# Performance work log

Measured on AMD Instinct MI355X. Metric: run time of the kernel, lower is better.

## Reference

```python
import jax, jax.numpy as jnp
import numpy as np

N = 116                      # AAL atlas nodes
E = N * (N - 1) // 2         # 6670 edges of the fully connected connectome
HID = 64
EDIM = 5
OUT = 4
ENC = HID + N // 2           # 122 raw brain-encoding features
EPS = 1e-10


def setup_inputs() -> dict:
    key = jax.random.key(0)
    ks = jax.random.split(key, 15)
    iu = np.triu_indices(N, k=1)                      # matches torch.nonzero(triu) order
    edge_index = jnp.asarray(np.stack(iu), dtype=jnp.int32)   # [2, E]
    rn = lambda k, s, sc=0.1: jax.random.normal(k, s, dtype=jnp.float32) * sc
    return dict(
        encoding_raw=rn(ks[0], (N, ENC), 1.0),
        edge_attr=rn(ks[1], (E, EDIM), 1.0),
        edge_index=edge_index,
        W_enc=rn(ks[2], (ENC, HID)), b_enc=rn(ks[3], (HID,)),
        W1=rn(ks[4], (HID, HID)), b1=rn(ks[5], (HID,)), p1=rn(ks[6], (1, EDIM)),
        We=rn(ks[7], (EDIM, EDIM)), be=rn(ks[8], (EDIM,)), pe=rn(ks[9], (1, HID)),
        W2=rn(ks[10], (HID, HID)), b2=rn(ks[11], (HID,)), p2=rn(ks[12], (1, EDIM)),
        Wl=rn(ks[13], (HID, OUT)), bl=rn(ks[14], (OUT,)),
    )


def _forward(encoding_raw, edge_attr, edge_index, W_enc, b_enc,
             W1, b1, p1, We, be, pe, W2, b2, p2, Wl, bl):
    eye_n = jnp.eye(N, dtype=jnp.float32)
    eye_e = jnp.eye(E, dtype=jnp.float32)
    adj_v = 1.0 - eye_n          # fully-connected node adjacency, zero diagonal
    adj_e = 1.0 - eye_e          # edge adjacency: ones minus eye
    # Incidence matrix T [N, E]: T[i,e] = T[j,e] = 1 for edge e = (i, j)
    cols = jnp.arange(E)
    T = (jnp.zeros((N, E), dtype=jnp.float32)
         .at[edge_index[0], cols].set(1.0)
         .at[edge_index[1], cols].set(1.0))

    # BrainEncoding: x = Linear(raw encoding)  (batch.x is None -> x = encodings)
    x = encoding_raw @ W_enc + b_enc                    # [N, HID]

    def node_conv(Hv, He, W, b, p):
        d = (He @ p.T)[:, 0]                            # [E] learned scalar per edge
        mult = (T * d) @ T.T                            # T diag(d) T^T  -> [N, N]
        # M1 = eye*1 + (1-eye)*mult, then * adj_v (zero diag) => mult * adj_v
        A = mult * adj_v
        return A @ (Hv @ W) + b

    def edge_conv(Hv, He, W, b, p):
        dv = (Hv @ p.T)[:, 0]                           # [N] learned scalar per node
        mult = T.T @ (dv[:, None] * T)                  # T^T diag(dv) T -> [E, E] dense
        A = mult * adj_e                                # M3 * adj_e => zero diag, off-diag mult
        A = A / (A.max(axis=0, keepdims=True) + EPS)    # column-max normalization
        return A @ (He @ W) + b

    # node_conv1 -> relu (dropout is identity in eval)
    x = jax.nn.relu(node_conv(x, edge_attr, W1, b1, p1))
    e = jax.nn.relu(edge_attr)
    # edge_conv1 -> relu
    e = jax.nn.relu(edge_conv(x, e, We, be, pe))
    x = jax.nn.relu(x)                                  # relu applied again (idempotent)
    # node_conv2 (no relu after)
    x = node_conv(x, e, W2, b2, p2)
    # global mean pool over the single graph, then classifier head
    pooled = jnp.mean(x, axis=0, keepdims=True)         # [1, HID]
    return pooled @ Wl + bl                             # [1, OUT]


def reference(encoding_raw, edge_attr, edge_index, W_enc, b_enc,
              W1, b1, p1, We, be, pe, W2, b2, p2, Wl, bl):
    return _forward(encoding_raw, edge_attr, edge_index, W_enc, b_enc,
                    W1, b1, p1, We, be, pe, W2, b2, p2, Wl, bl)
```

## Files before the change

kernel.cpp:

```cpp
#include <hip/hip_runtime.h>


#define NN   116
#define EE   6670
#define HID  64
#define EDIM 5
#define OUTD 4
#define ENC  122
#define EPSF 1e-10f
#define NH   (NN*HID)

__device__ __forceinline__ int eid_ij(int i, int j) {
    int a = i < j ? i : j;
    int b = i < j ? j : i;
    return a*NN - ((a*(a+1)) >> 1) + (b - a - 1);
}

__global__ __launch_bounds__(256) void kA(
    const float* __restrict__ enc, const float* __restrict__ ea,
    const float* __restrict__ W_enc, const float* __restrict__ b_enc,
    const float* __restrict__ p1, const float* __restrict__ We,
    const float* __restrict__ W1,
    float* __restrict__ Y1, float* __restrict__ d1, float* __restrict__ G)
{
    const int tid = threadIdx.x;
    if (blockIdx.x < 29) {
        __shared__ __align__(16) float sWe[ENC*HID];
        __shared__ __align__(16) float sW1[HID*HID];
        __shared__ __align__(16) float sEnc[4*ENC];
        __shared__ float sX[4*HID];
        {
            const float4* g4 = (const float4*)W_enc; float4* s4 = (float4*)sWe;
            for (int u = tid; u < ENC*HID/4; u += 256) s4[u] = g4[u];
        }
        {
            const float4* g4 = (const float4*)W1; float4* s4 = (float4*)sW1;
            for (int u = tid; u < HID*HID/4; u += 256) s4[u] = g4[u];
        }
        {
            const float4* g4 = (const float4*)(enc + blockIdx.x*4*ENC);
            float4* s4 = (float4*)sEnc;
            for (int u = tid; u < 4*ENC/4; u += 256) s4[u] = g4[u];
        }
        __syncthreads();
        const int w = tid >> 6, h = tid & 63;
        const int i = blockIdx.x*4 + w;
        float acc = b_enc[h];
        const float* er = sEnc + w*ENC;
        #pragma unroll 4
        for (int k = 0; k < ENC; ++k) acc = fmaf(er[k], sWe[k*HID + h], acc);
        sX[w*HID + h] = acc;
        __syncthreads();
        float a2 = 0.f;
        const float* xr = sX + w*HID;
        #pragma unroll 8
        for (int k = 0; k < HID; ++k) a2 = fmaf(xr[k], sW1[k*HID + h], a2);
        Y1[i*HID + h] = a2;
    } else {
        int u = (blockIdx.x - 29)*256 + tid;
        if (u < EE) {
            const float* r = ea + u*EDIM;
            float a0 = 0.f;
            #pragma unroll
            for (int k = 0; k < EDIM; ++k) a0 = fmaf(r[k], p1[k], a0);
            d1[u] = a0;
        } else if (u < EE + EE*EDIM) {
            int idx = u - EE;
            int e = idx / EDIM, k = idx - e*EDIM;
            const float* r = ea + e*EDIM;
            float a0 = 0.f;
            #pragma unroll
            for (int m = 0; m < EDIM; ++m) a0 = fmaf(fmaxf(r[m], 0.f), We[m*EDIM + k], a0);
            G[idx] = a0;
        }
    }
}

__global__ __launch_bounds__(256) void kB(
    const float* __restrict__ d1, const float* __restrict__ Y1,
    const float* __restrict__ b1, const float* __restrict__ pe,
    const float* __restrict__ W2,
    float* __restrict__ dv, float* __restrict__ Y2)
{
    __shared__ __align__(16) float sY[NH];
    __shared__ __align__(16) float sD[EE];
    __shared__ float sX2[4*HID];
    const int tid = threadIdx.x;
    {
        const float4* g4 = (const float4*)Y1; float4* s4 = (float4*)sY;
        for (int u = tid; u < NH/4; u += 256) s4[u] = g4[u];
        const float2* g2 = (const float2*)d1; float2* s2 = (float2*)sD;
        for (int u = tid; u < EE/2; u += 256) s2[u] = g2[u];
    }
    __syncthreads();
    const int w = tid >> 6, h = tid & 63;
    const int i = blockIdx.x*4 + w;
    float acc = b1[h];
    #pragma unroll 4
    for (int j = 0; j < NN; ++j) {
        int jj = (j == i) ? (j ^ 1) : j;
        float wgt = (j == i) ? 0.f : sD[eid_ij(i, jj)];
        acc = fmaf(wgt, sY[jj*HID + h], acc);
    }
    float v = fmaxf(acc, 0.f);
    float r = v * pe[h];
    #pragma unroll
    for (int off = 32; off > 0; off >>= 1) r += __shfl_down(r, off, 64);
    if (h == 0) dv[i] = r;
    sX2[w*HID + h] = v;
    __syncthreads();
    float a2 = 0.f;
    const float* xr = sX2 + w*HID;
    #pragma unroll 8
    for (int k = 0; k < HID; ++k) a2 = fmaf(xr[k], W2[k*HID + h], a2);
    Y2[i*HID + h] = a2;
}

__global__ __launch_bounds__(256) void kC(
    const float* __restrict__ G, const float* __restrict__ dv,
    float* __restrict__ S)
{
    const int wg = blockIdx.x*4 + (threadIdx.x >> 6);
    const int lane = threadIdx.x & 63;
    const int i = wg / EDIM, k = wg - i*EDIM;
    const float di = dv[i];
    float acc = 0.f;
    #pragma unroll
    for (int rep = 0; rep < 2; ++rep) {
        int j = lane + rep*64;
        if (j < NN && j != i) {
            float cm = fmaxf(fmaxf(di, dv[j]), 0.f) + EPSF;
            acc += G[eid_ij(i, j)*EDIM + k] / cm;
        }
    }
    #pragma unroll
    for (int off = 32; off > 0; off >>= 1) acc += __shfl_down(acc, off, 64);
    if (lane == 0) S[wg] = acc;
}

__global__ __launch_bounds__(256) void kD(
    const int* __restrict__ eidx, const float* __restrict__ G,
    const float* __restrict__ dv, const float* __restrict__ S,
    const float* __restrict__ be, const float* __restrict__ p2,
    float* __restrict__ d2, float* __restrict__ P)
{
    const int t = blockIdx.x*256 + threadIdx.x;
    if (blockIdx.x == 0 && threadIdx.x < HID) P[threadIdx.x] = 0.f;
    if (t >= EE) return;
    const int a = eidx[t], b = eidx[EE + t];
    const float da = dv[a], db = dv[b];
    const float rc = 1.f / (fmaxf(fmaxf(da, db), 0.f) + EPSF);
    float acc = 0.f;
    #pragma unroll
    for (int kk = 0; kk < EDIM; ++kk) {
        float gp = G[t*EDIM + kk] * rc;
        float v = fmaf(da, S[a*EDIM + kk] - gp, fmaf(db, S[b*EDIM + kk] - gp, be[kk]));
        acc = fmaf(fmaxf(v, 0.f), p2[kk], acc);
    }
    d2[t] = acc;
}

__global__ __launch_bounds__(256) void kE(
    const float* __restrict__ d2, const float* __restrict__ Y2,
    const float* __restrict__ b2, float* __restrict__ P)
{
    __shared__ __align__(16) float sY[NH];
    __shared__ __align__(16) float sD[EE];
    __shared__ float sR[4*HID];
    const int tid = threadIdx.x;
    {
        const float4* g4 = (const float4*)Y2; float4* s4 = (float4*)sY;
        for (int u = tid; u < NH/4; u += 256) s4[u] = g4[u];
        const float2* g2 = (const float2*)d2; float2* s2 = (float2*)sD;
        for (int u = tid; u < EE/2; u += 256) s2[u] = g2[u];
    }
    __syncthreads();
    const int w = tid >> 6, h = tid & 63;
    const int i = blockIdx.x*4 + w;
    float acc = b2[h];
    #pragma unroll 4
    for (int j = 0; j < NN; ++j) {
        int jj = (j == i) ? (j ^ 1) : j;
        float wgt = (j == i) ? 0.f : sD[eid_ij(i, jj)];
        acc = fmaf(wgt, sY[jj*HID + h], acc);
    }
    sR[w*HID + h] = acc;
    __syncthreads();
    if (w == 0) {
        float s4 = sR[h] + sR[HID + h] + sR[2*HID + h] + sR[3*HID + h];
        atomicAdd(&P[h], s4);
    }
}

__global__ void kF(const float* __restrict__ P, const float* __restrict__ Wl,
                   const float* __restrict__ bl, float* __restrict__ out)
{
    const int lane = threadIdx.x;
    float val = P[lane] * (1.0f / NN);
    float res[OUTD];
    #pragma unroll
    for (int o = 0; o < OUTD; ++o) {
        float r = val * Wl[lane*OUTD + o];
        #pragma unroll
        for (int off = 32; off > 0; off >>= 1) r += __shfl_xor(r, off, 64);
        res[o] = r;
    }
    if (lane < OUTD) out[lane] = res[lane] + bl[lane];
}

extern "C" void kernel_launch(void* const* d_in, const int* in_sizes, int n_in,
                              void* d_out, int out_size, void* d_ws, size_t ws_size,
                              hipStream_t stream)
{
    const float* enc   = (const float*)d_in[0];
    const float* ea    = (const float*)d_in[1];
    const int*   eidx  = (const int*)  d_in[2];
    const float* W_enc = (const float*)d_in[3];
    const float* b_enc = (const float*)d_in[4];
    const float* W1    = (const float*)d_in[5];
    const float* b1    = (const float*)d_in[6];
    const float* p1    = (const float*)d_in[7];
    const float* We    = (const float*)d_in[8];
    const float* be    = (const float*)d_in[9];
    const float* pe    = (const float*)d_in[10];
    const float* W2    = (const float*)d_in[11];
    const float* b2    = (const float*)d_in[12];
    const float* p2    = (const float*)d_in[13];
    const float* Wl    = (const float*)d_in[14];
    const float* bl    = (const float*)d_in[15];
    float* ws = (float*)d_ws;

    float* Y1 = ws;
    float* P  = ws;
    float* Y2 = ws + NH;
    float* dA = ws + 2*NH;
    float* G  = dA + EE;
    float* dv = G + EE*EDIM;
    float* S  = dv + NN;
    float* out = (float*)d_out;

    kA<<<29 + (EE + EE*EDIM + 255)/256, 256, 0, stream>>>(enc, ea, W_enc, b_enc, p1, We, W1, Y1, dA, G);
    kB<<<29, 256, 0, stream>>>(dA, Y1, b1, pe, W2, dv, Y2);
    kC<<<(NN*EDIM)/4, 256, 0, stream>>>(G, dv, S);
    kD<<<(EE + 255)/256, 256, 0, stream>>>(eidx, G, dv, S, be, p2, dA, P);
    kE<<<29, 256, 0, stream>>>(dA, Y2, b2, P);
    kF<<<1, 64, 0, stream>>>(P, Wl, bl, out);
}
```

Measured before the change: 124.2 us.

## Fuse six kernels into one persistent kernel with atomic grid barriers

Replaces the six-kernel chain with a single 29-block persistent kernel whose stages are separated by software grid barriers built on atomic counters reset by a memset. This targets the per-launch overhead and inter-kernel gaps of a small, latency-bound pipeline. In exchange the elementwise stages run on only 29 blocks instead of many, and the first-stage weights are read straight from global memory rather than staged in LDS. Correctness also depends on all 29 blocks being co-resident for the spin barriers to make progress.

After: 149.7 us. 20.5% more time.

```diff
diff --git a/kernel.cpp b/kernel.cpp
--- a/kernel.cpp
+++ b/kernel.cpp
@@ -9,6 +9,7 @@
 #define ENC  122
 #define EPSF 1e-10f
 #define NH   (NN*HID)
+#define NB   29
 
 __device__ __forceinline__ int eid_ij(int i, int j) {
     int a = i < j ? i : j;
@@ -16,196 +17,179 @@
     return a*NN - ((a*(a+1)) >> 1) + (b - a - 1);
 }
 
-__global__ __launch_bounds__(256) void kA(
+__device__ __forceinline__ void gridbar(unsigned* bar, unsigned target) {
+    __syncthreads();
+    if (threadIdx.x == 0) {
+        __threadfence();
+        atomicAdd(bar, 1u);
+        while (__hip_atomic_load(bar, __ATOMIC_RELAXED, __HIP_MEMORY_SCOPE_AGENT) < target)
+            __builtin_amdgcn_s_sleep(2);
+        __threadfence();
+    }
+    __syncthreads();
+}
+
+__global__ __launch_bounds__(256) void fused(
     const float* __restrict__ enc, const float* __restrict__ ea,
+    const int* __restrict__ eidx,
     const float* __restrict__ W_enc, const float* __restrict__ b_enc,
+    const float* __restrict__ W1, const float* __restrict__ b1,
     const float* __restrict__ p1, const float* __restrict__ We,
-    const float* __restrict__ W1,
-    float* __restrict__ Y1, float* __restrict__ d1, float* __restrict__ G)
-{
-    const int tid = threadIdx.x;
-    if (blockIdx.x < 29) {
-        __shared__ __align__(16) float sWe[ENC*HID];
-        __shared__ __align__(16) float sW1[HID*HID];
-        __shared__ __align__(16) float sEnc[4*ENC];
-        __shared__ float sX[4*HID];
-        {
-            const float4* g4 = (const float4*)W_enc; float4* s4 = (float4*)sWe;
-            for (int u = tid; u < ENC*HID/4; u += 256) s4[u] = g4[u];
-        }
-        {
-            const float4* g4 = (const float4*)W1; float4* s4 = (float4*)sW1;
-            for (int u = tid; u < HID*HID/4; u += 256) s4[u] = g4[u];
-        }
-        {
-            const float4* g4 = (const float4*)(enc + blockIdx.x*4*ENC);
-            float4* s4 = (float4*)sEnc;
-            for (int u = tid; u < 4*ENC/4; u += 256) s4[u] = g4[u];
-        }
-        __syncthreads();
-        const int w = tid >> 6, h = tid & 63;
-        const int i = blockIdx.x*4 + w;
-        float acc = b_enc[h];
-        const float* er = sEnc + w*ENC;
-        #pragma unroll 4
-        for (int k = 0; k < ENC; ++k) acc = fmaf(er[k], sWe[k*HID + h], acc);
-        sX[w*HID + h] = acc;
-        __syncthreads();
-        float a2 = 0.f;
-        const float* xr = sX + w*HID;
-        #pragma unroll 8
-        for (int k = 0; k < HID; ++k) a2 = fmaf(xr[k], sW1[k*HID + h], a2);
-        Y1[i*HID + h] = a2;
-    } else {
-        int u = (blockIdx.x - 29)*256 + tid;
-        if (u < EE) {
-            const float* r = ea + u*EDIM;
-            float a0 = 0.f;
-            #pragma unroll
-            for (int k = 0; k < EDIM; ++k) a0 = fmaf(r[k], p1[k], a0);
-            d1[u] = a0;
-        } else if (u < EE + EE*EDIM) {
-            int idx = u - EE;
-            int e = idx / EDIM, k = idx - e*EDIM;
-            const float* r = ea + e*EDIM;
-            float a0 = 0.f;
-            #pragma unroll
-            for (int m = 0; m < EDIM; ++m) a0 = fmaf(fmaxf(r[m], 0.f), We[m*EDIM + k], a0);
-            G[idx] = a0;
-        }
-    }
-}
-
-__global__ __launch_bounds__(256) void kB(
-    const float* __restrict__ d1, const float* __restrict__ Y1,
-    const float* __restrict__ b1, const float* __restrict__ pe,
-    const float* __restrict__ W2,
-    float* __restrict__ dv, float* __restrict__ Y2)
+    const float* __restrict__ be, const float* __restrict__ pe,
+    const float* __restrict__ W2, const float* __restrict__ b2,
+    const float* __restrict__ p2, const float* __restrict__ Wl,
+    const float* __restrict__ bl,
+    float* __restrict__ Y1, float* __restrict__ Y2,
+    float* __restrict__ d1, float* __restrict__ d2,
+    float* __restrict__ G,  float* __restrict__ dv,
+    float* __restrict__ S,  float* __restrict__ P,
+    unsigned* __restrict__ bar,
+    float* __restrict__ out)
 {
     __shared__ __align__(16) float sY[NH];
     __shared__ __align__(16) float sD[EE];
-    __shared__ float sX2[4*HID];
-    const int tid = threadIdx.x;
+    __shared__ float sRow[4*HID];
+    const int tid  = threadIdx.x;
+    const int w    = tid >> 6, lane = tid & 63;
+    const int node = blockIdx.x*4 + w;
+    const int gt   = blockIdx.x*256 + tid;
+
+    {
+        float x = b_enc[lane];
+        const float* er = enc + node*ENC;
+        #pragma unroll 4
+        for (int k = 0; k < ENC; ++k) x = fmaf(er[k], W_enc[k*HID + lane], x);
+        sRow[w*HID + lane] = x;
+        __syncthreads();
+        float y = 0.f;
+        const float* xr = sRow + w*HID;
+        #pragma unroll 8
+        for (int k = 0; k < HID; ++k) y = fmaf(xr[k], W1[k*HID + lane], y);
+        Y1[node*HID + lane] = y;
+
+        for (int u = gt; u < EE + EE*EDIM; u += NB*256) {
+            if (u < EE) {
+                const float* r = ea + u*EDIM;
+                float a0 = 0.f;
+                #pragma unroll
+                for (int k = 0; k < EDIM; ++k) a0 = fmaf(r[k], p1[k], a0);
+                d1[u] = a0;
+            } else {
+                int idx = u - EE;
+                int e = idx / EDIM, k = idx - e*EDIM;
+                const float* r = ea + e*EDIM;
+                float a0 = 0.f;
+                #pragma unroll
+                for (int m = 0; m < EDIM; ++m) a0 = fmaf(fmaxf(r[m], 0.f), We[m*EDIM + k], a0);
+                G[idx] = a0;
+            }
+        }
+        if (gt < HID) P[gt] = 0.f;
+    }
+    gridbar(bar + 0, NB);
+
     {
         const float4* g4 = (const float4*)Y1; float4* s4 = (float4*)sY;
         for (int u = tid; u < NH/4; u += 256) s4[u] = g4[u];
         const float2* g2 = (const float2*)d1; float2* s2 = (float2*)sD;
         for (int u = tid; u < EE/2; u += 256) s2[u] = g2[u];
-    }
-    __syncthreads();
-    const int w = tid >> 6, h = tid & 63;
-    const int i = blockIdx.x*4 + w;
-    float acc = b1[h];
-    #pragma unroll 4
-    for (int j = 0; j < NN; ++j) {
-        int jj = (j == i) ? (j ^ 1) : j;
-        float wgt = (j == i) ? 0.f : sD[eid_ij(i, jj)];
-        acc = fmaf(wgt, sY[jj*HID + h], acc);
-    }
-    float v = fmaxf(acc, 0.f);
-    float r = v * pe[h];
-    #pragma unroll
-    for (int off = 32; off > 0; off >>= 1) r += __shfl_down(r, off, 64);
-    if (h == 0) dv[i] = r;
-    sX2[w*HID + h] = v;
-    __syncthreads();
-    float a2 = 0.f;
-    const float* xr = sX2 + w*HID;
-    #pragma unroll 8
-    for (int k = 0; k < HID; ++k) a2 = fmaf(xr[k], W2[k*HID + h], a2);
-    Y2[i*HID + h] = a2;
-}
-
-__global__ __launch_bounds__(256) void kC(
-    const float* __restrict__ G, const float* __restrict__ dv,
-    float* __restrict__ S)
-{
-    const int wg = blockIdx.x*4 + (threadIdx.x >> 6);
-    const int lane = threadIdx.x & 63;
-    const int i = wg / EDIM, k = wg - i*EDIM;
-    const float di = dv[i];
-    float acc = 0.f;
-    #pragma unroll
-    for (int rep = 0; rep < 2; ++rep) {
-        int j = lane + rep*64;
-        if (j < NN && j != i) {
-            float cm = fmaxf(fmaxf(di, dv[j]), 0.f) + EPSF;
-            acc += G[eid_ij(i, j)*EDIM + k] / cm;
-        }
-    }
-    #pragma unroll
-    for (int off = 32; off > 0; off >>= 1) acc += __shfl_down(acc, off, 64);
-    if (lane == 0) S[wg] = acc;
-}
-
-__global__ __launch_bounds__(256) void kD(
-    const int* __restrict__ eidx, const float* __restrict__ G,
-    const float* __restrict__ dv, const float* __restrict__ S,
-    const float* __restrict__ be, const float* __restrict__ p2,
-    float* __restrict__ d2, float* __restrict__ P)
-{
-    const int t = blockIdx.x*256 + threadIdx.x;
-    if (blockIdx.x == 0 && threadIdx.x < HID) P[threadIdx.x] = 0.f;
-    if (t >= EE) return;
-    const int a = eidx[t], b = eidx[EE + t];
-    const float da = dv[a], db = dv[b];
-    const float rc = 1.f / (fmaxf(fmaxf(da, db), 0.f) + EPSF);
-    float acc = 0.f;
-    #pragma unroll
-    for (int kk = 0; kk < EDIM; ++kk) {
-        float gp = G[t*EDIM + kk] * rc;
-        float v = fmaf(da, S[a*EDIM + kk] - gp, fmaf(db, S[b*EDIM + kk] - gp, be[kk]));
-        acc = fmaf(fmaxf(v, 0.f), p2[kk], acc);
-    }
-    d2[t] = acc;
-}
-
-__global__ __launch_bounds__(256) void kE(
-    const float* __restrict__ d2, const float* __restrict__ Y2,
-    const float* __restrict__ b2, float* __restrict__ P)
-{
-    __shared__ __align__(16) float sY[NH];
-    __shared__ __align__(16) float sD[EE];
-    __shared__ float sR[4*HID];
-    const int tid = threadIdx.x;
+        __syncthreads();
+        float acc = b1[lane];
+        #pragma unroll 4
+        for (int j = 0; j < NN; ++j) {
+            int jj = (j == node) ? (j ^ 1) : j;
+            float wgt = (j == node) ? 0.f : sD[eid_ij(node, jj)];
+            acc = fmaf(wgt, sY[jj*HID + lane], acc);
+        }
+        float v = fmaxf(acc, 0.f);
+        float r = v * pe[lane];
+        #pragma unroll
+        for (int off = 32; off > 0; off >>= 1) r += __shfl_xor(r, off, 64);
+        if (lane == 0) dv[node] = r;
+        __syncthreads();
+        sRow[w*HID + lane] = v;
+        __syncthreads();
+        float y = 0.f;
+        const float* xr = sRow + w*HID;
+        #pragma unroll 8
+        for (int k = 0; k < HID; ++k) y = fmaf(xr[k], W2[k*HID + lane], y);
+        Y2[node*HID + lane] = y;
+    }
+    gridbar(bar + 1, NB);
+
+    {
+        if (tid < NN) sRow[tid] = dv[tid];
+        __syncthreads();
+        #pragma unroll
+        for (int rep = 0; rep < EDIM; ++rep) {
+            int p = node + rep*NN;
+            int i = p / EDIM, k = p - i*EDIM;
+            float di = sRow[i];
+            float acc = 0.f;
+            #pragma unroll
+            for (int half = 0; half < 2; ++half) {
+                int j = lane + half*64;
+                if (j < NN && j != i) {
+                    float cm = fmaxf(fmaxf(di, sRow[j]), 0.f) + EPSF;
+                    acc += G[eid_ij(i, j)*EDIM + k] / cm;
+                }
+            }
+            #pragma unroll
+            for (int off = 32; off > 0; off >>= 1) acc += __shfl_xor(acc, off, 64);
+            if (lane == 0) S[p] = acc;
+        }
+    }
+    gridbar(bar + 2, NB);
+
+    if (gt < EE) {
+        const int a = eidx[gt], b = eidx[EE + gt];
+        const float da = sRow[a], db = sRow[b];
+        const float rc = 1.f / (fmaxf(fmaxf(da, db), 0.f) + EPSF);
+        float acc = 0.f;
+        #pragma unroll
+        for (int kk = 0; kk < EDIM; ++kk) {
+            float gp = G[gt*EDIM + kk] * rc;
+            float v = fmaf(da, S[a*EDIM + kk] - gp, fmaf(db, S[b*EDIM + kk] - gp, be[kk]));
+            acc = fmaf(fmaxf(v, 0.f), p2[kk], acc);
+        }
+        d2[gt] = acc;
+    }
+    gridbar(bar + 3, NB);
+
     {
         const float4* g4 = (const float4*)Y2; float4* s4 = (float4*)sY;
         for (int u = tid; u < NH/4; u += 256) s4[u] = g4[u];
         const float2* g2 = (const float2*)d2; float2* s2 = (float2*)sD;
         for (int u = tid; u < EE/2; u += 256) s2[u] = g2[u];
-    }
-    __syncthreads();
-    const int w = tid >> 6, h = tid & 63;
-    const int i = blockIdx.x*4 + w;
-    float acc = b2[h];
-    #pragma unroll 4
-    for (int j = 0; j < NN; ++j) {
-        int jj = (j == i) ? (j ^ 1) : j;
-        float wgt = (j == i) ? 0.f : sD[eid_ij(i, jj)];
-        acc = fmaf(wgt, sY[jj*HID + h], acc);
-    }
-    sR[w*HID + h] = acc;
-    __syncthreads();
-    if (w == 0) {
-        float s4 = sR[h] + sR[HID + h] + sR[2*HID + h] + sR[3*HID + h];
-        atomicAdd(&P[h], s4);
-    }
-}
-
-__global__ void kF(const float* __restrict__ P, const float* __restrict__ Wl,
-                   const float* __restrict__ bl, float* __restrict__ out)
-{
-    const int lane = threadIdx.x;
-    float val = P[lane] * (1.0f / NN);
-    float res[OUTD];
-    #pragma unroll
-    for (int o = 0; o < OUTD; ++o) {
-        float r = val * Wl[lane*OUTD + o];
-        #pragma unroll
-        for (int off = 32; off > 0; off >>= 1) r += __shfl_xor(r, off, 64);
-        res[o] = r;
-    }
-    if (lane < OUTD) out[lane] = res[lane] + bl[lane];
+        __syncthreads();
+        float acc = b2[lane];
+        #pragma unroll 4
+        for (int j = 0; j < NN; ++j) {
+            int jj = (j == node) ? (j ^ 1) : j;
+            float wgt = (j == node) ? 0.f : sD[eid_ij(node, jj)];
+            acc = fmaf(wgt, sY[jj*HID + lane], acc);
+        }
+        sRow[w*HID + lane] = acc;
+        __syncthreads();
+        if (w == 0) {
+            float s4v = sRow[lane] + sRow[HID + lane] + sRow[2*HID + lane] + sRow[3*HID + lane];
+            atomicAdd(&P[lane], s4v);
+        }
+    }
+    gridbar(bar + 4, NB);
+
+    if (blockIdx.x == 0 && w == 0) {
+        float val = P[lane] * (1.0f / NN);
+        float res[OUTD];
+        #pragma unroll
+        for (int o = 0; o < OUTD; ++o) {
+            float r = val * Wl[lane*OUTD + o];
+            #pragma unroll
+            for (int off = 32; off > 0; off >>= 1) r += __shfl_xor(r, off, 64);
+            res[o] = r;
+        }
+        if (lane < OUTD) out[lane] = res[lane] + bl[lane];
+    }
 }
 
 extern "C" void kernel_launch(void* const* d_in, const int* in_sizes, int n_in,
@@ -231,18 +215,18 @@
     float* ws = (float*)d_ws;
 
     float* Y1 = ws;
-    float* P  = ws;
-    float* Y2 = ws + NH;
-    float* dA = ws + 2*NH;
-    float* G  = dA + EE;
-    float* dv = G + EE*EDIM;
-    float* S  = dv + NN;
+    float* Y2 = ws + 7424;
+    float* d1 = ws + 14848;
+    float* d2 = ws + 21520;
+    float* G  = ws + 28192;
+    float* dv = ws + 61544;
+    float* S  = ws + 61664;
+    float* P  = ws + 62248;
+    unsigned* bar = (unsigned*)(ws + 62312);
     float* out = (float*)d_out;
 
-    kA<<<29 + (EE + EE*EDIM + 255)/256, 256, 0, stream>>>(enc, ea, W_enc, b_enc, p1, We, W1, Y1, dA, G);
-    kB<<<29, 256, 0, stream>>>(dA, Y1, b1, pe, W2, dv, Y2);
-    kC<<<(NN*EDIM)/4, 256, 0, stream>>>(G, dv, S);
-    kD<<<(EE + 255)/256, 256, 0, stream>>>(eidx, G, dv, S, be, p2, dA, P);
-    kE<<<29, 256, 0, stream>>>(dA, Y2, b2, P);
-    kF<<<1, 64, 0, stream>>>(P, Wl, bl, out);
-}
+    hipMemsetAsync(bar, 0, 5*sizeof(unsigned), stream);
+    fused<<<NB, 256, 0, stream>>>(enc, ea, eidx, W_enc, b_enc, W1, b1, p1, We,
+                                  be, pe, W2, b2, p2, Wl, bl,
+                                  Y1, Y2, d1, d2, G, dv, S, P, bar, out);
+}
```
